# Performance work log

Measured on AMD Instinct MI355X. Metric: run time of the kernel, lower is better.

## Reference

```python
import jax, jax.numpy as jnp
import numpy as np

DIMS = 64
D_MODEL = 1024

def setup_inputs() -> dict:
    key = jax.random.key(0)
    ks = jax.random.split(key, 8)
    B, Sk, Sq = 4, 4096, 2048
    enc = jax.random.normal(ks[0], (B, Sk, D_MODEL), dtype=jnp.float32)
    dec = jax.random.normal(ks[1], (B, Sq, D_MODEL), dtype=jnp.float32)
    s = 1.0 / np.sqrt(D_MODEL)
    Wq = jax.random.normal(ks[2], (D_MODEL, DIMS), dtype=jnp.float32) * s
    Wk = jax.random.normal(ks[3], (D_MODEL, DIMS), dtype=jnp.float32) * s
    Wv = jax.random.normal(ks[4], (D_MODEL, DIMS), dtype=jnp.float32) * s
    bq = jnp.zeros((DIMS,), jnp.float32)
    bk = jnp.zeros((DIMS,), jnp.float32)
    bv = jnp.zeros((DIMS,), jnp.float32)
    return {"encoder_output": enc, "decoder": dec, "Wq": Wq, "bq": bq,
            "Wk": Wk, "bk": bk, "Wv": Wv, "bv": bv}

def reference(encoder_output, decoder, Wq, bq, Wk, bk, Wv, bv):
    # q: [B,Sq,dims], k/v: [B,Sk,dims]
    q = decoder @ Wq + bq
    k = encoder_output @ Wk + bk
    v = encoder_output @ Wv + bv
    scale = DIMS ** (-0.5)
    scores = jnp.einsum('bqd,bkd->bqk', q, k) * scale  # [B,Sq,Sk]
    attn = jax.nn.softmax(scores, axis=-1)
    out = jnp.einsum('bqk,bkd->bqd', attn, v)  # [B,Sq,dims]
    return out
```

## Files before the change

### kernel.cpp

```cpp
#include <hip/hip_runtime.h>
#include <hip/hip_bf16.h>

typedef __attribute__((ext_vector_type(8))) short short8;
typedef __attribute__((ext_vector_type(4))) float f32x4;
typedef __attribute__((ext_vector_type(16))) float f32x16;
typedef unsigned short u16;

#define L2E 1.4426950408889634f

__device__ __forceinline__ u16 f2bf(float x) {
    union { float f; unsigned u; } v; v.f = x;
    return (u16)((v.u + 0x7FFFu + ((v.u >> 16) & 1u)) >> 16);
}

__device__ __forceinline__ void gl_lds16(const void* g, void* l) {
    __builtin_amdgcn_global_load_lds(
        (const __attribute__((address_space(1))) unsigned int*)g,
        (__attribute__((address_space(3))) unsigned int*)l, 16, 0, 0);
}

__device__ __forceinline__ int cvtpk(float lo, float hi) {
    int r;
    asm("v_cvt_pk_bf16_f32 %0, %1, %2" : "=v"(r) : "v"(lo), "v"(hi));
    return r;
}

__device__ __forceinline__ void plswap(int& a, int& b) {
    asm volatile("v_permlane32_swap_b32 %0, %1" : "+v"(a), "+v"(b));
}

#define WTQ_OFF   0
#define WTKV_OFF  131072
#define Q_OFF     393216
#define K_OFF     1441792
#define VT_OFF    3538944
#define OPT_OFF   5636096

__global__ __launch_bounds__(256) void prep2(
    const float* __restrict__ Wq, const float* __restrict__ Wk,
    const float* __restrict__ Wv, u16* __restrict__ wtq, u16* __restrict__ wtkv)
{
    __shared__ u16 tile[64][66];
    const int t = threadIdx.x;
    const int mat = blockIdx.x >> 4, kc = blockIdx.x & 15;
    const float* src = (mat == 0) ? Wq : ((mat == 1) ? Wk : Wv);
    u16* dst = (mat == 0) ? wtq : (wtkv + ((mat == 2) ? 64 * 1024 : 0));
    #pragma unroll
    for (int c = 0; c < 4; ++c) {
        int id = t + c * 256;
        int r = id >> 4, c4 = id & 15;
        float4 v = *(const float4*)(src + (size_t)(kc * 64 + r) * 64 + c4 * 4);
        tile[r][c4 * 4 + 0] = f2bf(v.x);
        tile[r][c4 * 4 + 1] = f2bf(v.y);
        tile[r][c4 * 4 + 2] = f2bf(v.z);
        tile[r][c4 * 4 + 3] = f2bf(v.w);
    }
    __syncthreads();
    int n = t >> 2, kch = t & 3;
    short8 v0, v1;
    #pragma unroll
    for (int j = 0; j < 8; ++j) {
        v0[j] = (short)tile[kch * 16 + j][n];
        v1[j] = (short)tile[kch * 16 + 8 + j][n];
    }
    u16* dp = dst + (size_t)n * 1024 + kc * 64 + kch * 16;
    *(short8*)dp = v0;
    *(short8*)(dp + 8) = v1;
}

__global__ __launch_bounds__(256) void proj3(
    const float* __restrict__ enc, const float* __restrict__ dec,
    const u16* __restrict__ wtkv, const u16* __restrict__ wtq,
    const float* __restrict__ bk, const float* __restrict__ bv,
    const float* __restrict__ bq,
    u16* __restrict__ Kb, u16* __restrict__ Vtb, u16* __restrict__ Qb)
{
    constexpr int ABYTES = 32 * 64 * 4;
    constexpr int WBYTES = 128 * 64 * 2;
    constexpr int BUF = ABYTES + WBYTES;
    __shared__ __align__(16) char lds[2 * BUF];

    const int t = threadIdx.x, l = t & 63, w = t >> 6;
    const int wm = w >> 1, wn = w & 1;
    const bool is_enc = blockIdx.x < 512;
    const int r0 = is_enc ? blockIdx.x * 32 : (blockIdx.x - 512) * 32;
    const float* A = is_enc ? enc : dec;
    const u16* Wsrc = is_enc ? wtkv : wtq;

    f32x4 acc[4];
    #pragma unroll
    for (int n = 0; n < 4; ++n) acc[n] = (f32x4){0.f, 0.f, 0.f, 0.f};

    auto stage = [&](int buf, int kt) {
        char* Ab = lds + buf * BUF;
        char* Wb = Ab + ABYTES;
        const int k0 = kt * 64;
        #pragma unroll
        for (int c = 0; c < 2; ++c) {
            int id = t + c * 256;
            int row = id >> 4, sl = id & 15;
            gl_lds16(A + (size_t)(r0 + row) * 1024 + k0 + ((sl ^ (row & 7)) << 2),
                     Ab + id * 16);
        }
        #pragma unroll
        for (int c = 0; c < 4; ++c) {
            int id = t + c * 256;
            int row = id >> 3, sl = id & 7;
            int wr = is_enc ? row : (row & 63);
            gl_lds16(Wsrc + (size_t)wr * 1024 + k0 + ((sl ^ (row & 7)) << 3),
                     Wb + id * 16);
        }
    };

    stage(0, 0);
    __syncthreads();
    int cur = 0;
    for (int kt = 0; kt < 16; ++kt) {
        if (kt < 15) stage(cur ^ 1, kt + 1);
        const char* Ab = lds + cur * BUF;
        const char* Wb = Ab + ABYTES;
        #pragma unroll
        for (int ks = 0; ks < 2; ++ks) {
            int arow = wm * 16 + (l & 15);
            int s0 = ks * 8 + (l >> 4) * 2;
            f32x4 lo = *(const f32x4*)(Ab + arow * 256 + ((s0 ^ (arow & 7)) << 4));
            f32x4 hi = *(const f32x4*)(Ab + arow * 256 + (((s0 + 1) ^ (arow & 7)) << 4));
            short8 afr;
            afr[0] = (short)f2bf(lo[0]); afr[1] = (short)f2bf(lo[1]);
            afr[2] = (short)f2bf(lo[2]); afr[3] = (short)f2bf(lo[3]);
            afr[4] = (short)f2bf(hi[0]); afr[5] = (short)f2bf(hi[1]);
            afr[6] = (short)f2bf(hi[2]); afr[7] = (short)f2bf(hi[3]);
            #pragma unroll
            for (int n = 0; n < 4; ++n) {
                int wrow = wn * 64 + n * 16 + (l & 15);
                int c8 = ks * 4 + (l >> 4);
                short8 bfr = *(const short8*)(Wb + wrow * 128 + ((c8 ^ (wrow & 7)) << 4));
                acc[n] = __builtin_amdgcn_mfma_f32_16x16x32_bf16(afr, bfr, acc[n], 0, 0, 0);
            }
        }
        __syncthreads();
        cur ^= 1;
    }

    u16* Vs2 = (u16*)lds;
    if (is_enc) {
        if (wn == 0) {
            #pragma unroll
            for (int n = 0; n < 4; ++n) {
                int col = n * 16 + (l & 15);
                #pragma unroll
                for (int i = 0; i < 4; ++i) {
                    int lrow = wm * 16 + (l >> 4) * 4 + i;
                    Kb[(size_t)(r0 + lrow) * 64 + col] = f2bf(acc[n][i] + bk[col]);
                }
            }
        } else {
            #pragma unroll
            for (int n = 0; n < 4; ++n) {
                int d = n * 16 + (l & 15);
                #pragma unroll
                for (int i = 0; i < 4; ++i) {
                    int lrow = wm * 16 + (l >> 4) * 4 + i;
                    Vs2[lrow * 66 + d] = f2bf(acc[n][i] + bv[d]);
                }
            }
        }
        __syncthreads();
        int d = t >> 2, sch = t & 3;
        short8 v;
        #pragma unroll
        for (int j = 0; j < 8; ++j) v[j] = (short)Vs2[(sch * 8 + j) * 66 + d];
        int bb = r0 >> 12, s0r = r0 & 4095;
        *(short8*)(Vtb + ((size_t)(bb * 64 + d)) * 4096 + s0r + sch * 8) = v;
    } else {
        if (wn == 0) {
            #pragma unroll
            for (int n = 0; n < 4; ++n) {
                int col = n * 16 + (l & 15);
                #pragma unroll
                for (int i = 0; i < 4; ++i) {
                    int lrow = wm * 16 + (l >> 4) * 4 + i;
                    Qb[(size_t)(r0 + lrow) * 64 + col] =
                        f2bf((acc[n][i] + bq[col]) * 0.125f);
                }
            }
        }
    }
}

template<int NS>
__global__ __launch_bounds__(256, 2) void attn3(
    const u16* __restrict__ Qb, const u16* __restrict__ Kb,
    const u16* __restrict__ Vtb, float* __restrict__ OpT,
    float* __restrict__ Mpart, float* __restrict__ Lpart)
{
    constexpr int SPAN = 4096 / NS;
    constexpr int NIT = SPAN / 64;
    const int t = threadIdx.x, l = t & 63, w = t >> 6;
    const int b = blockIdx.y, bz = blockIdx.z;
    const int q0 = (blockIdx.x * 4 + w) * 32;
    const int lq = l & 31, lh = l >> 5;

    short8 qf[4];
    #pragma unroll
    for (int dt = 0; dt < 4; ++dt)
        qf[dt] = *(const short8*)(Qb + (size_t)(b * 2048 + q0 + lq) * 64
                                  + dt * 16 + lh * 8);

    f32x16 o0, o1;
    #pragma unroll
    for (int r = 0; r < 16; ++r) { o0[r] = 0.f; o1[r] = 0.f; }
    float mrun = -INFINITY, lrun = 0.f;

    const size_t kbase = (size_t)b * 4096 * 64;
    const size_t vbase = (size_t)b * 64 * 4096;

    auto LOADT = [&](short8 (&kf)[4], short8 (&vf)[2][2], int kt) {
        #pragma unroll
        for (int dt = 0; dt < 4; ++dt)
            kf[dt] = *(const short8*)(Kb + kbase + (size_t)(kt + lq) * 64
                                      + dt * 16 + lh * 8);
        #pragma unroll
        for (int db = 0; db < 2; ++db)
            #pragma unroll
            for (int kh = 0; kh < 2; ++kh)
                vf[db][kh] = *(const short8*)(Vtb + vbase
                                              + (size_t)(db * 32 + lq) * 4096
                                              + kt + kh * 16 + lh * 8);
    };

    auto COMPUTE = [&](short8 (&kf)[4], short8 (&vf)[2][2]) {
        f32x16 s;
        #pragma unroll
        for (int r = 0; r < 16; ++r) s[r] = 0.f;
        #pragma unroll
        for (int dt = 0; dt < 4; ++dt)
            s = __builtin_amdgcn_mfma_f32_32x32x16_bf16(kf[dt], qf[dt], s, 0, 0, 0);
        float m0 = fmaxf(fmaxf(s[0], s[1]), fmaxf(s[2], s[3]));
        float m1 = fmaxf(fmaxf(s[4], s[5]), fmaxf(s[6], s[7]));
        float m2 = fmaxf(fmaxf(s[8], s[9]), fmaxf(s[10], s[11]));
        float m3 = fmaxf(fmaxf(s[12], s[13]), fmaxf(s[14], s[15]));
        float pm = fmaxf(fmaxf(m0, m1), fmaxf(m2, m3));
        pm = fmaxf(pm, __shfl_xor(pm, 32));
        float mn = fmaxf(mrun, pm);
        float corr = exp2f((mrun - mn) * L2E);
        mrun = mn;
        float nm = -mn * L2E;
        float p[16];
        #pragma unroll
        for (int r = 0; r < 16; ++r) p[r] = exp2f(fmaf(s[r], L2E, nm));
        float rs = ((p[0] + p[1]) + (p[2] + p[3])) + ((p[4] + p[5]) + (p[6] + p[7]))
                 + ((p[8] + p[9]) + (p[10] + p[11])) + ((p[12] + p[13]) + (p[14] + p[15]));
        rs += __shfl_xor(rs, 32);
        lrun = lrun * corr + rs;
        o0 *= corr;
        o1 *= corr;
        short8 pb[2];
        #pragma unroll
        for (int kh = 0; kh < 2; ++kh) {
            int a0 = cvtpk(p[kh * 8 + 0], p[kh * 8 + 1]);
            int b0 = cvtpk(p[kh * 8 + 4], p[kh * 8 + 5]);
            int a1 = cvtpk(p[kh * 8 + 2], p[kh * 8 + 3]);
            int b1 = cvtpk(p[kh * 8 + 6], p[kh * 8 + 7]);
            plswap(a0, b0);
            plswap(a1, b1);
            union { int wd[4]; short8 v; } u;
            u.wd[0] = a0; u.wd[1] = a1; u.wd[2] = b0; u.wd[3] = b1;
            pb[kh] = u.v;
        }
        #pragma unroll
        for (int kh = 0; kh < 2; ++kh) {
            o0 = __builtin_amdgcn_mfma_f32_32x32x16_bf16(vf[0][kh], pb[kh], o0, 0, 0, 0);
            o1 = __builtin_amdgcn_mfma_f32_32x32x16_bf16(vf[1][kh], pb[kh], o1, 0, 0, 0);
        }
    };

    short8 kfA[4], vfA[2][2], kfB[4], vfB[2][2];
    const int kt0 = bz * SPAN;
    LOADT(kfA, vfA, kt0);
    for (int it = 0; it < NIT; ++it) {
        const int kt = kt0 + it * 64;
        LOADT(kfB, vfB, kt + 32);
        COMPUTE(kfA, vfA);
        if (it < NIT - 1) LOADT(kfA, vfA, kt + 64);
        COMPUTE(kfB, vfB);
    }

    const size_t obase = ((size_t)(bz * 4 + b) * 64) * 2048 + q0 + lq;
    #pragma unroll
    for (int r = 0; r < 16; ++r) {
        int drow = (r & 3) + 8 * (r >> 2) + 4 * lh;
        OpT[obase + (size_t)drow * 2048] = o0[r];
        OpT[obase + (size_t)(drow + 32) * 2048] = o1[r];
    }
    if (l < 32) {
        Mpart[bz * 8192 + b * 2048 + q0 + l] = mrun;
        Lpart[bz * 8192 + b * 2048 + q0 + l] = lrun;
    }
}

template<int NS>
__global__ __launch_bounds__(256) void combine3(
    const float* __restrict__ OpT, const float* __restrict__ Mpart,
    const float* __restrict__ Lpart, float* __restrict__ Out)
{
    __shared__ float wsh[NS][32];
    __shared__ float trans[32][72];
    const int t = threadIdx.x;
    const int b = blockIdx.x >> 6;
    const int q0 = (blockIdx.x & 63) * 32;

    if (t < 32) {
        int q = t;
        float m4[NS], M = -INFINITY;
        #pragma unroll
        for (int ks = 0; ks < NS; ++ks) {
            m4[ks] = Mpart[ks * 8192 + b * 2048 + q0 + q];
            M = fmaxf(M, m4[ks]);
        }
        float wv[NS], Lf = 0.f;
        #pragma unroll
        for (int ks = 0; ks < NS; ++ks) {
            wv[ks] = exp2f((m4[ks] - M) * L2E);
            Lf += Lpart[ks * 8192 + b * 2048 + q0 + q] * wv[ks];
        }
        float inv = 1.0f / Lf;
        #pragma unroll
        for (int ks = 0; ks < NS; ++ks) wsh[ks][q] = wv[ks] * inv;
    }
    __syncthreads();
    {
        int d = t >> 2, qc = (t & 3) * 8;
        float a8[8];
        #pragma unroll
        for (int j = 0; j < 8; ++j) a8[j] = 0.f;
        #pragma unroll
        for (int ks = 0; ks < NS; ++ks) {
            const float* p = OpT + (((size_t)(ks * 4 + b)) * 64 + d) * 2048 + q0 + qc;
            f32x4 x = *(const f32x4*)p;
            f32x4 y = *(const f32x4*)(p + 4);
            #pragma unroll
            for (int j = 0; j < 4; ++j) {
                a8[j]     += x[j] * wsh[ks][qc + j];
                a8[4 + j] += y[j] * wsh[ks][qc + 4 + j];
            }
        }
        #pragma unroll
        for (int j = 0; j < 8; ++j) trans[qc + j][d] = a8[j];
    }
    __syncthreads();
    {
        int q = t >> 3, dc = (t & 7) * 8;
        f32x4 x = *(const f32x4*)&trans[q][dc];
        f32x4 y = *(const f32x4*)&trans[q][dc + 4];
        float* dst = Out + ((size_t)(b * 2048 + q0 + q)) * 64 + dc;
        *(f32x4*)dst = x;
        *(f32x4*)(dst + 4) = y;
    }
}

extern "C" void kernel_launch(void* const* d_in, const int* in_sizes, int n_in,
                              void* d_out, int out_size, void* d_ws, size_t ws_size,
                              hipStream_t stream) {
    const float* enc = (const float*)d_in[0];
    const float* dec = (const float*)d_in[1];
    const float* Wq  = (const float*)d_in[2];
    const float* bq  = (const float*)d_in[3];
    const float* Wk  = (const float*)d_in[4];
    const float* bk  = (const float*)d_in[5];
    const float* Wv  = (const float*)d_in[6];
    const float* bv  = (const float*)d_in[7];

    char* ws = (char*)d_ws;
    u16* wtq   = (u16*)(ws + WTQ_OFF);
    u16* wtkv  = (u16*)(ws + WTKV_OFF);
    u16* Qb    = (u16*)(ws + Q_OFF);
    u16* Kb    = (u16*)(ws + K_OFF);
    u16* Vtb   = (u16*)(ws + VT_OFF);
    float* OpT = (float*)(ws + OPT_OFF);

    prep2<<<48, 256, 0, stream>>>(Wq, Wk, Wv, wtq, wtkv);
    proj3<<<768, 256, 0, stream>>>(enc, dec, wtkv, wtq, bk, bv, bq, Kb, Vtb, Qb);

    const size_t need8 = (size_t)OPT_OFF + 8ull * 4 * 64 * 2048 * 4 + 2ull * 8 * 8192 * 4;
    if (ws_size >= need8) {
        float* Mpart = (float*)(ws + OPT_OFF + 8ull * 4 * 64 * 2048 * 4);
        float* Lpart = Mpart + 8 * 8192;
        attn3<8><<<dim3(16, 4, 8), 256, 0, stream>>>(Qb, Kb, Vtb, OpT, Mpart, Lpart);
        combine3<8><<<256, 256, 0, stream>>>(OpT, Mpart, Lpart, (float*)d_out);
    } else {
        float* Mpart = (float*)(ws + OPT_OFF + 4ull * 4 * 64 * 2048 * 4);
        float* Lpart = Mpart + 4 * 8192;
        attn3<4><<<dim3(16, 4, 4), 256, 0, stream>>>(Qb, Kb, Vtb, OpT, Mpart, Lpart);
        combine3<4><<<256, 256, 0, stream>>>(OpT, Mpart, Lpart, (float*)d_out);
    }
}
```

Before: 179.7 us.

## Replace LDS-staged projection GEMM with direct-register per-wave loads

The projection kernel no longer double-buffers input and weight tiles through LDS with global_load_lds. Each wave now owns 16 rows and loads fp32 activations and bf16 weights straight from global memory into MFMA fragments, covering all 128 K/V output columns per wave. V is written transposed using 4-element packed stores instead of an LDS transpose. This removes LDS traffic and block barriers, and the grid shrinks to 384 blocks with an occupancy hint of 2. In exchange, weights are re-read from global memory by every wave and the per-lane loads are less coalesced.

```diff
diff --git a/kernel.cpp b/kernel.cpp
--- a/kernel.cpp
+++ b/kernel.cpp
@@ -2,6 +2,7 @@
 #include <hip/hip_bf16.h>
 
 typedef __attribute__((ext_vector_type(8))) short short8;
+typedef __attribute__((ext_vector_type(4))) short short4_;
 typedef __attribute__((ext_vector_type(4))) float f32x4;
 typedef __attribute__((ext_vector_type(16))) float f32x16;
 typedef unsigned short u16;
@@ -11,12 +12,6 @@
 __device__ __forceinline__ u16 f2bf(float x) {
     union { float f; unsigned u; } v; v.f = x;
     return (u16)((v.u + 0x7FFFu + ((v.u >> 16) & 1u)) >> 16);
-}
-
-__device__ __forceinline__ void gl_lds16(const void* g, void* l) {
-    __builtin_amdgcn_global_load_lds(
-        (const __attribute__((address_space(1))) unsigned int*)g,
-        (__attribute__((address_space(3))) unsigned int*)l, 16, 0, 0);
 }
 
 __device__ __forceinline__ int cvtpk(float lo, float hi) {
@@ -68,123 +63,81 @@
     *(short8*)(dp + 8) = v1;
 }
 
-__global__ __launch_bounds__(256) void proj3(
+template<int NREP>
+__device__ __forceinline__ void proj5_body(
+    const float* __restrict__ A, const u16* __restrict__ W,
+    const float* __restrict__ bias0, const float* __restrict__ bias1,
+    float scale, u16* __restrict__ out0, u16* __restrict__ Vtb,
+    int r0, int l)
+{
+    const int arow = l & 15, q = l >> 4;
+    f32x4 acc[NREP];
+    #pragma unroll
+    for (int n = 0; n < NREP; ++n) acc[n] = (f32x4){0.f, 0.f, 0.f, 0.f};
+
+    const float* ap = A + (size_t)(r0 + arow) * 1024 + q * 8;
+    const u16* wp0 = W + (size_t)arow * 1024 + q * 8;
+
+    #pragma unroll 4
+    for (int i = 0; i < 16; ++i) {
+        short8 af[2];
+        #pragma unroll
+        for (int ks = 0; ks < 2; ++ks) {
+            f32x4 lo = *(const f32x4*)(ap + i * 64 + ks * 32);
+            f32x4 hi = *(const f32x4*)(ap + i * 64 + ks * 32 + 4);
+            short8 r;
+            r[0] = (short)f2bf(lo[0]); r[1] = (short)f2bf(lo[1]);
+            r[2] = (short)f2bf(lo[2]); r[3] = (short)f2bf(lo[3]);
+            r[4] = (short)f2bf(hi[0]); r[5] = (short)f2bf(hi[1]);
+            r[6] = (short)f2bf(hi[2]); r[7] = (short)f2bf(hi[3]);
+            af[ks] = r;
+        }
+        #pragma unroll
+        for (int n = 0; n < NREP; ++n) {
+            const u16* wp = wp0 + (size_t)n * 16384 + i * 64;
+            short8 w0 = *(const short8*)wp;
+            short8 w1 = *(const short8*)(wp + 32);
+            acc[n] = __builtin_amdgcn_mfma_f32_16x16x32_bf16(af[0], w0, acc[n], 0, 0, 0);
+            acc[n] = __builtin_amdgcn_mfma_f32_16x16x32_bf16(af[1], w1, acc[n], 0, 0, 0);
+        }
+    }
+
+    #pragma unroll
+    for (int n = 0; n < NREP; ++n) {
+        int col = n * 16 + arow;
+        if (NREP == 4 || n < 4) {
+            float bv0 = bias0[col];
+            #pragma unroll
+            for (int i = 0; i < 4; ++i) {
+                int row = q * 4 + i;
+                out0[(size_t)(r0 + row) * 64 + col] = f2bf((acc[n][i] + bv0) * scale);
+            }
+        } else {
+            int d = col - 64;
+            float bv1 = bias1[d];
+            short4_ pk;
+            #pragma unroll
+            for (int i = 0; i < 4; ++i) pk[i] = (short)f2bf(acc[n][i] + bv1);
+            int bb = r0 >> 12, sbase = (r0 & 4095) + q * 4;
+            *(short4_*)(Vtb + (size_t)(bb * 64 + d) * 4096 + sbase) = pk;
+        }
+    }
+}
+
+__global__ __launch_bounds__(256, 2) void proj5(
     const float* __restrict__ enc, const float* __restrict__ dec,
     const u16* __restrict__ wtkv, const u16* __restrict__ wtq,
     const float* __restrict__ bk, const float* __restrict__ bv,
     const float* __restrict__ bq,
     u16* __restrict__ Kb, u16* __restrict__ Vtb, u16* __restrict__ Qb)
 {
-    constexpr int ABYTES = 32 * 64 * 4;
-    constexpr int WBYTES = 128 * 64 * 2;
-    constexpr int BUF = ABYTES + WBYTES;
-    __shared__ __align__(16) char lds[2 * BUF];
-
     const int t = threadIdx.x, l = t & 63, w = t >> 6;
-    const int wm = w >> 1, wn = w & 1;
-    const bool is_enc = blockIdx.x < 512;
-    const int r0 = is_enc ? blockIdx.x * 32 : (blockIdx.x - 512) * 32;
-    const float* A = is_enc ? enc : dec;
-    const u16* Wsrc = is_enc ? wtkv : wtq;
-
-    f32x4 acc[4];
-    #pragma unroll
-    for (int n = 0; n < 4; ++n) acc[n] = (f32x4){0.f, 0.f, 0.f, 0.f};
-
-    auto stage = [&](int buf, int kt) {
-        char* Ab = lds + buf * BUF;
-        char* Wb = Ab + ABYTES;
-        const int k0 = kt * 64;
-        #pragma unroll
-        for (int c = 0; c < 2; ++c) {
-            int id = t + c * 256;
-            int row = id >> 4, sl = id & 15;
-            gl_lds16(A + (size_t)(r0 + row) * 1024 + k0 + ((sl ^ (row & 7)) << 2),
-                     Ab + id * 16);
-        }
-        #pragma unroll
-        for (int c = 0; c < 4; ++c) {
-            int id = t + c * 256;
-            int row = id >> 3, sl = id & 7;
-            int wr = is_enc ? row : (row & 63);
-            gl_lds16(Wsrc + (size_t)wr * 1024 + k0 + ((sl ^ (row & 7)) << 3),
-                     Wb + id * 16);
-        }
-    };
-
-    stage(0, 0);
-    __syncthreads();
-    int cur = 0;
-    for (int kt = 0; kt < 16; ++kt) {
-        if (kt < 15) stage(cur ^ 1, kt + 1);
-        const char* Ab = lds + cur * BUF;
-        const char* Wb = Ab + ABYTES;
-        #pragma unroll
-        for (int ks = 0; ks < 2; ++ks) {
-            int arow = wm * 16 + (l & 15);
-            int s0 = ks * 8 + (l >> 4) * 2;
-            f32x4 lo = *(const f32x4*)(Ab + arow * 256 + ((s0 ^ (arow & 7)) << 4));
-            f32x4 hi = *(const f32x4*)(Ab + arow * 256 + (((s0 + 1) ^ (arow & 7)) << 4));
-            short8 afr;
-            afr[0] = (short)f2bf(lo[0]); afr[1] = (short)f2bf(lo[1]);
-            afr[2] = (short)f2bf(lo[2]); afr[3] = (short)f2bf(lo[3]);
-            afr[4] = (short)f2bf(hi[0]); afr[5] = (short)f2bf(hi[1]);
-            afr[6] = (short)f2bf(hi[2]); afr[7] = (short)f2bf(hi[3]);
-            #pragma unroll
-            for (int n = 0; n < 4; ++n) {
-                int wrow = wn * 64 + n * 16 + (l & 15);
-                int c8 = ks * 4 + (l >> 4);
-                short8 bfr = *(const short8*)(Wb + wrow * 128 + ((c8 ^ (wrow & 7)) << 4));
-                acc[n] = __builtin_amdgcn_mfma_f32_16x16x32_bf16(afr, bfr, acc[n], 0, 0, 0);
-            }
-        }
-        __syncthreads();
-        cur ^= 1;
-    }
-
-    u16* Vs2 = (u16*)lds;
-    if (is_enc) {
-        if (wn == 0) {
-            #pragma unroll
-            for (int n = 0; n < 4; ++n) {
-                int col = n * 16 + (l & 15);
-                #pragma unroll
-                for (int i = 0; i < 4; ++i) {
-                    int lrow = wm * 16 + (l >> 4) * 4 + i;
-                    Kb[(size_t)(r0 + lrow) * 64 + col] = f2bf(acc[n][i] + bk[col]);
-                }
-            }
-        } else {
-            #pragma unroll
-            for (int n = 0; n < 4; ++n) {
-                int d = n * 16 + (l & 15);
-                #pragma unroll
-                for (int i = 0; i < 4; ++i) {
-                    int lrow = wm * 16 + (l >> 4) * 4 + i;
-                    Vs2[lrow * 66 + d] = f2bf(acc[n][i] + bv[d]);
-                }
-            }
-        }
-        __syncthreads();
-        int d = t >> 2, sch = t & 3;
-        short8 v;
-        #pragma unroll
-        for (int j = 0; j < 8; ++j) v[j] = (short)Vs2[(sch * 8 + j) * 66 + d];
-        int bb = r0 >> 12, s0r = r0 & 4095;
-        *(short8*)(Vtb + ((size_t)(bb * 64 + d)) * 4096 + s0r + sch * 8) = v;
+    if (blockIdx.x < 256) {
+        int r0 = blockIdx.x * 64 + w * 16;
+        proj5_body<8>(enc, wtkv, bk, bv, 1.0f, Kb, Vtb, r0, l);
     } else {
-        if (wn == 0) {
-            #pragma unroll
-            for (int n = 0; n < 4; ++n) {
-                int col = n * 16 + (l & 15);
-                #pragma unroll
-                for (int i = 0; i < 4; ++i) {
-                    int lrow = wm * 16 + (l >> 4) * 4 + i;
-                    Qb[(size_t)(r0 + lrow) * 64 + col] =
-                        f2bf((acc[n][i] + bq[col]) * 0.125f);
-                }
-            }
-        }
+        int r0 = (blockIdx.x - 256) * 64 + w * 16;
+        proj5_body<4>(dec, wtq, bq, bq, 0.125f, Qb, (u16*)nullptr, r0, l);
     }
 }
 
@@ -380,7 +333,7 @@
     float* OpT = (float*)(ws + OPT_OFF);
 
     prep2<<<48, 256, 0, stream>>>(Wq, Wk, Wv, wtq, wtkv);
-    proj3<<<768, 256, 0, stream>>>(enc, dec, wtkv, wtq, bk, bv, bq, Kb, Vtb, Qb);
+    proj5<<<384, 256, 0, stream>>>(enc, dec, wtkv, wtq, bk, bv, bq, Kb, Vtb, Qb);
 
     const size_t need8 = (size_t)OPT_OFF + 8ull * 4 * 64 * 2048 * 4 + 2ull * 8 * 8192 * 4;
     if (ws_size >= need8) {
```

After: 216.0 us. +20.2%, slower.
